# Optimization experiments

Hardware: AMD Instinct MI355X
Metric: run time of the kernel (lower is better)

The kernel has to match this reference:

```python
import jax, jax.numpy as jnp
import numpy as np

D_MODEL = 512
NUM_HEADS = 8


def setup_inputs() -> dict:
    key = jax.random.key(0)
    ks = jax.random.split(key, 12)
    B, S, D = 2, 4096, D_MODEL
    s = 1.0 / np.sqrt(D)
    return {
        "q": jax.random.normal(ks[0], (B, S, D), jnp.float32),
        "k": jax.random.normal(ks[1], (B, S, D), jnp.float32),
        "v": jax.random.normal(ks[2], (B, S, D), jnp.float32),
        "w_q": jax.random.normal(ks[3], (D, D), jnp.float32) * s,
        "b_q": jax.random.normal(ks[4], (D,), jnp.float32) * s,
        "w_k": jax.random.normal(ks[5], (D, D), jnp.float32) * s,
        "b_k": jax.random.normal(ks[6], (D,), jnp.float32) * s,
        "w_v": jax.random.normal(ks[7], (D, D), jnp.float32) * s,
        "b_v": jax.random.normal(ks[8], (D,), jnp.float32) * s,
        "w_o": jax.random.normal(ks[9], (D, D), jnp.float32) * s,
        "b_o": jax.random.normal(ks[10], (D,), jnp.float32) * s,
    }


def _split(x, num_heads):
    B, S, D = x.shape
    return x.reshape(B, S, num_heads, D // num_heads).transpose(0, 2, 1, 3)


def reference(q, k, v, w_q, b_q, w_k, b_k, w_v, b_v, w_o, b_o):
    # Linear projections (torch Linear: x @ W^T + b)
    qp = q @ w_q.T + b_q
    kp = k @ w_k.T + b_k
    vp = v @ w_v.T + b_v
    # split into heads: [B, H, S, d_head]
    qh = _split(qp, NUM_HEADS)
    kh = _split(kp, NUM_HEADS)
    vh = _split(vp, NUM_HEADS)
    d_head = qh.shape[-1]
    # NOTE: original scales by sqrt(d_model of the per-head tensor) == sqrt(d_head)
    score = jnp.einsum("bhqd,bhkd->bhqk", qh, kh) / jnp.sqrt(jnp.float32(d_head))
    attn = jax.nn.softmax(score, axis=-1)  # full [B,H,S,S] materialized, as in source
    out = jnp.einsum("bhqk,bhkd->bhqd", attn, vh)
    # concat heads back to [B, S, D]
    B, H, S, Dh = out.shape
    out = out.transpose(0, 2, 1, 3).reshape(B, S, H * Dh)
    return out @ w_o.T + b_o
```

## Files before the change

kernel.cpp:

```cpp
#include <hip/hip_runtime.h>
#include <math.h>

typedef __bf16 bf16_t;
typedef __bf16 bf16x4_v __attribute__((ext_vector_type(4)));
typedef __bf16 bf16x8_t __attribute__((ext_vector_type(8)));
typedef float f32x4_t __attribute__((ext_vector_type(4)));
typedef unsigned uint2_t __attribute__((ext_vector_type(2)));
typedef unsigned uint4_t __attribute__((ext_vector_type(4)));

#define S_LEN 4096
#define DM 512
#define NH 8
#define DH 64
#define MTOT 8192

#define Q_SCALE 0.1803368801111204f

#define REG   4194304
#define WREG  262144
#define W_OFF (3 * REG)
#define CVT_TOTAL (3 * REG + 4 * WREG)
#define QH_OFF CVT_TOTAL

__device__ inline f32x4_t mfma16(bf16x8_t a, bf16x8_t b, f32x4_t c) {
    return __builtin_amdgcn_mfma_f32_16x16x32_bf16(a, b, c, 0, 0, 0);
}

__device__ inline unsigned pkbf16(float a, float b) {
    unsigned short ra = __builtin_bit_cast(unsigned short, (bf16_t)a);
    unsigned short rb = __builtin_bit_cast(unsigned short, (bf16_t)b);
    return (unsigned)ra | ((unsigned)rb << 16);
}

__device__ inline void async_copy16(const void* g, void* l) {
    __builtin_amdgcn_global_load_lds(
        (const __attribute__((address_space(1))) void*)g,
        (__attribute__((address_space(3))) void*)l, 16, 0, 0);
}

__global__ __launch_bounds__(256) void cvt_all(
    const float* __restrict__ q, const float* __restrict__ k, const float* __restrict__ v,
    const float* __restrict__ wq, const float* __restrict__ wk,
    const float* __restrict__ wv, const float* __restrict__ wo,
    bf16_t* __restrict__ dst)
{
    long gidx = (long)blockIdx.x * 2048 + (long)threadIdx.x * 8;
    const float* src;
    long off = gidx;
    if      (gidx < 1L * REG)          { src = q; }
    else if (gidx < 2L * REG)          { src = k;  off = gidx - 1L * REG; }
    else if (gidx < 3L * REG)          { src = v;  off = gidx - 2L * REG; }
    else if (gidx < W_OFF + 1L * WREG) { src = wq; off = gidx - W_OFF; }
    else if (gidx < W_OFF + 2L * WREG) { src = wk; off = gidx - (W_OFF + 1L * WREG); }
    else if (gidx < W_OFF + 3L * WREG) { src = wv; off = gidx - (W_OFF + 2L * WREG); }
    else                               { src = wo; off = gidx - (W_OFF + 3L * WREG); }
    float4 a = *(const float4*)(src + off);
    float4 b = *(const float4*)(src + off + 4);
    bf16x8_t h;
    h[0] = (bf16_t)a.x; h[1] = (bf16_t)a.y; h[2] = (bf16_t)a.z; h[3] = (bf16_t)a.w;
    h[4] = (bf16_t)b.x; h[5] = (bf16_t)b.y; h[6] = (bf16_t)b.z; h[7] = (bf16_t)b.w;
    *(bf16x8_t*)(dst + gidx) = h;
}

__global__ __launch_bounds__(256) void gemm_qkv(
    const bf16_t* __restrict__ XWb,
    const float* __restrict__ B0, const float* __restrict__ B1, const float* __restrict__ B2,
    bf16_t* __restrict__ dst_base)
{
    const int p = blockIdx.z;
    const bf16_t* __restrict__ X = XWb + (size_t)p * REG;
    const bf16_t* __restrict__ W = XWb + W_OFF + (size_t)p * WREG;
    const float* __restrict__ Bi = (p == 0) ? B0 : ((p == 1) ? B1 : B2);
    bf16_t* __restrict__ dst = dst_base + (size_t)p * REG;

    const int m0 = blockIdx.x * 128;
    const int n0 = blockIdx.y * 128;
    const int tid = threadIdx.x;
    const int lane = tid & 63, wid = tid >> 6;
    const int lm = lane & 15, lg = lane >> 4;
    const int wm = (wid >> 1) * 64, wn = (wid & 1) * 64;

    __shared__ __align__(16) bf16_t As[128 * 64];
    __shared__ __align__(16) bf16_t Bs[128 * 64];

    f32x4_t acc[4][4] = {};

    const int r0 = tid >> 3, c7 = tid & 7;
    const int cA0 = ((lg) ^ (lm & 7)) * 8;
    const int cA1 = ((4 + lg) ^ (lm & 7)) * 8;

    for (int kb = 0; kb < DM / 64; ++kb) {
        const int k0 = kb * 64;
#pragma unroll
        for (int i = 0; i < 4; ++i) {
            int row = i * 32 + r0;
            int ch = c7 ^ (row & 7);
            async_copy16(X + (size_t)(m0 + row) * DM + k0 + ch * 8, (char*)As + (i * 256 + tid) * 16);
            async_copy16(W + (size_t)(n0 + row) * DM + k0 + ch * 8, (char*)Bs + (i * 256 + tid) * 16);
        }
        __syncthreads();
#pragma unroll
        for (int kd = 0; kd < 2; ++kd) {
            const int co = kd ? cA1 : cA0;
            bf16x8_t fa[4], fb[4];
#pragma unroll
            for (int mt = 0; mt < 4; ++mt) {
                fa[mt] = *(const bf16x8_t*)(As + (wm + mt * 16 + lm) * 64 + co);
                fb[mt] = *(const bf16x8_t*)(Bs + (wn + mt * 16 + lm) * 64 + co);
            }
            if (p < 2) {
#pragma unroll
                for (int mt = 0; mt < 4; ++mt)
#pragma unroll
                    for (int nt = 0; nt < 4; ++nt)
                        acc[nt][mt] = mfma16(fb[nt], fa[mt], acc[nt][mt]);
            } else {
#pragma unroll
                for (int mt = 0; mt < 4; ++mt)
#pragma unroll
                    for (int nt = 0; nt < 4; ++nt)
                        acc[mt][nt] = mfma16(fa[mt], fb[nt], acc[mt][nt]);
            }
        }
        __syncthreads();
    }

    if (p == 2) {
#pragma unroll
        for (int nt = 0; nt < 4; ++nt) {
            int col = n0 + wn + nt * 16 + lm;
            float bv = Bi[col];
            int h = (col >> 6) & 7, dc = col & 63;
#pragma unroll
            for (int mt = 0; mt < 4; ++mt) {
                int mrow = m0 + wm + mt * 16 + lg * 4;
                int bb = mrow >> 12, s = mrow & (S_LEN - 1);
                bf16x4_v pk;
#pragma unroll
                for (int r = 0; r < 4; ++r) pk[r] = (bf16_t)(acc[mt][nt][r] + bv);
                *(bf16x4_v*)&dst[(((size_t)(bb * NH + h)) * DH + dc) * S_LEN + s] = pk;
            }
        }
    } else {
        const float scale = (p == 0) ? Q_SCALE : 1.0f;
#pragma unroll
        for (int nt = 0; nt < 4; ++nt) {
            int ncol = n0 + wn + nt * 16 + lg * 4;
            float4 bv4 = *(const float4*)&Bi[ncol];
            int h = (ncol >> 6) & 7, dc = ncol & 63;
#pragma unroll
            for (int mt = 0; mt < 4; ++mt) {
                int m = m0 + wm + mt * 16 + lm;
                int bb = m >> 12, s = m & (S_LEN - 1);
                bf16x4_v pk;
                pk[0] = (bf16_t)((acc[nt][mt][0] + bv4.x) * scale);
                pk[1] = (bf16_t)((acc[nt][mt][1] + bv4.y) * scale);
                pk[2] = (bf16_t)((acc[nt][mt][2] + bv4.z) * scale);
                pk[3] = (bf16_t)((acc[nt][mt][3] + bv4.w) * scale);
                *(bf16x4_v*)&dst[(((size_t)(bb * NH + h)) * S_LEN + s) * DH + dc] = pk;
            }
        }
    }
}

__global__ __launch_bounds__(256, 2) void flash_attn(
    const bf16_t* __restrict__ Qh, const bf16_t* __restrict__ Kh,
    const bf16_t* __restrict__ Vth, bf16_t* __restrict__ O)
{
    const int bh = blockIdx.y;
    const int q0 = blockIdx.x * 128;
    const int tid = threadIdx.x;
    const int lane = tid & 63, wid = tid >> 6;
    const int lm = lane & 15, lg = lane >> 4;
    const int qg = wid & 1;
    const int kvh = wid >> 1;

    const bf16_t* __restrict__ Qb  = Qh  + (size_t)bh * S_LEN * DH;
    const bf16_t* __restrict__ Kb  = Kh  + (size_t)bh * S_LEN * DH;
    const bf16_t* __restrict__ Vtg = Vth + (size_t)bh * S_LEN * DH;

    __shared__ __align__(16) char smem[65536];

    bf16x8_t bQ[4][2];
#pragma unroll
    for (int nt = 0; nt < 4; ++nt)
#pragma unroll
        for (int kd = 0; kd < 2; ++kd)
            bQ[nt][kd] = *(const bf16x8_t*)(Qb + (size_t)(q0 + qg * 64 + nt * 16 + lm) * DH + kd * 32 + lg * 8);

    f32x4_t o_acc[4][4] = {};
    float l_acc[4] = {0.f, 0.f, 0.f, 0.f};

    const int srow = tid >> 3;
    const int slch = (tid & 7) ^ (srow & 7);
    const bf16_t* gK = Kb + (size_t)srow * DH + slch * 8;
    const bf16_t* gV = Vtg + (size_t)srow * S_LEN + slch * 8;

    const int cK0 = ((lg) ^ (lm & 7)) * 16;
    const int cK1 = ((4 + lg) ^ (lm & 7)) * 16;

    {
        char* b = smem;
#pragma unroll
        for (int i = 0; i < 4; ++i)
            async_copy16(gK + (size_t)(32 * i) * DH, b + i * 4096 + tid * 16);
#pragma unroll
        for (int i = 0; i < 4; ++i)
            async_copy16(gV + (size_t)(i & 1) * 32 * S_LEN + (i >> 1) * 64,
                         b + 16384 + i * 4096 + tid * 16);
    }

    const int NT = S_LEN / 128;
    for (int it = 0; it < NT; ++it) {
        const char* buf = smem + (it & 1) * 32768;
        __syncthreads();

        if (it + 1 < NT) {
            char* nb = smem + ((it + 1) & 1) * 32768;
            const int kvb = (it + 1) * 128;
#pragma unroll
            for (int i = 0; i < 4; ++i)
                async_copy16(gK + (size_t)(kvb + 32 * i) * DH, nb + i * 4096 + tid * 16);
#pragma unroll
            for (int i = 0; i < 4; ++i)
                async_copy16(gV + (size_t)(i & 1) * 32 * S_LEN + kvb + (i >> 1) * 64,
                             nb + 16384 + i * 4096 + tid * 16);
        }

        const char* ksb = buf + kvh * 8192;
        const char* vsb = buf + 16384 + kvh * 8192;

        unsigned pk[4][4][2];
#pragma unroll
        for (int mt = 0; mt < 4; ++mt) {
            const char* krow = ksb + (mt * 16 + lm) * 128;
            bf16x8_t aK0 = *(const bf16x8_t*)(krow + cK0);
            bf16x8_t aK1 = *(const bf16x8_t*)(krow + cK1);
#pragma unroll
            for (int nt = 0; nt < 4; ++nt) {
                f32x4_t s = {};
                s = mfma16(aK0, bQ[nt][0], s);
                s = mfma16(aK1, bQ[nt][1], s);
                float e0 = __builtin_amdgcn_exp2f(s[0]);
                float e1 = __builtin_amdgcn_exp2f(s[1]);
                float e2 = __builtin_amdgcn_exp2f(s[2]);
                float e3 = __builtin_amdgcn_exp2f(s[3]);
                pk[mt][nt][0] = pkbf16(e0, e1);
                pk[mt][nt][1] = pkbf16(e2, e3);
                l_acc[nt] += (e0 + e1) + (e2 + e3);
            }
        }

#pragma unroll
        for (int mt = 0; mt < 4; ++mt) {
            const char* vrow = vsb + (mt * 16 + lm) * 128;
#pragma unroll
            for (int cc = 0; cc < 2; ++cc) {
                const int ca = 2 * cc, cb = 2 * cc + 1;
                int pc0 = (ca * 2 + (lg >> 1)) ^ (lm & 7);
                int pc1 = (cb * 2 + (lg >> 1)) ^ (lm & 7);
                uint2_t va0 = *(const uint2_t*)(vrow + pc0 * 16 + (lg & 1) * 8);
                uint2_t va1 = *(const uint2_t*)(vrow + pc1 * 16 + (lg & 1) * 8);
                bf16x8_t vA = __builtin_bit_cast(bf16x8_t, (uint4_t){va0[0], va0[1], va1[0], va1[1]});
#pragma unroll
                for (int nt = 0; nt < 4; ++nt) {
                    bf16x8_t bP = __builtin_bit_cast(bf16x8_t,
                        (uint4_t){pk[ca][nt][0], pk[ca][nt][1], pk[cb][nt][0], pk[cb][nt][1]});
                    o_acc[mt][nt] = mfma16(vA, bP, o_acc[mt][nt]);
                }
            }
        }
    }

#pragma unroll
    for (int nt = 0; nt < 4; ++nt) {
        l_acc[nt] += __shfl_xor(l_acc[nt], 16, 64);
        l_acc[nt] += __shfl_xor(l_acc[nt], 32, 64);
    }

    __syncthreads();

    float* ob = (float*)smem + qg * (64 * 68);
    float* lb = (float*)(smem + 34816);

    if (kvh == 1) {
#pragma unroll
        for (int nt = 0; nt < 4; ++nt) {
#pragma unroll
            for (int mt = 0; mt < 4; ++mt)
                *(f32x4_t*)&ob[(nt * 16 + lm) * 68 + mt * 16 + lg * 4] = o_acc[mt][nt];
            if (lg == 0) lb[qg * 64 + nt * 16 + lm] = l_acc[nt];
        }
    }
    __syncthreads();
    if (kvh == 0) {
        const int bb = bh >> 3, h = bh & 7;
#pragma unroll
        for (int nt = 0; nt < 4; ++nt) {
            float ltot = l_acc[nt] + lb[qg * 64 + nt * 16 + lm];
            float inv = 1.0f / ltot;
            int q = q0 + qg * 64 + nt * 16 + lm;
            size_t base = ((size_t)(bb * S_LEN + q)) * DM + h * DH;
#pragma unroll
            for (int mt = 0; mt < 4; ++mt) {
                f32x4_t orow = *(const f32x4_t*)&ob[(nt * 16 + lm) * 68 + mt * 16 + lg * 4];
                bf16x4_v pkd;
#pragma unroll
                for (int r = 0; r < 4; ++r)
                    pkd[r] = (bf16_t)((o_acc[mt][nt][r] + orow[r]) * inv);
                *(bf16x4_v*)&O[base + mt * 16 + lg * 4] = pkd;
            }
        }
    }
}

__global__ __launch_bounds__(256) void gemm_out(
    const bf16_t* __restrict__ A, const bf16_t* __restrict__ W,
    const float* __restrict__ Bi, float* __restrict__ out)
{
    const int m0 = blockIdx.x * 64;
    const int n0 = blockIdx.y * 128;
    const int tid = threadIdx.x;
    const int lane = tid & 63, wid = tid >> 6;
    const int lm = lane & 15, lg = lane >> 4;
    const int wm = (wid >> 1) * 32, wn = (wid & 1) * 64;

    __shared__ __align__(16) bf16_t As[64 * 64];
    __shared__ __align__(16) bf16_t Bs[128 * 64];

    f32x4_t acc[4][2] = {};

    const int r0 = tid >> 3, c7 = tid & 7;
    const int cA0 = ((lg) ^ (lm & 7)) * 8;
    const int cA1 = ((4 + lg) ^ (lm & 7)) * 8;

    for (int kb = 0; kb < DM / 64; ++kb) {
        const int k0 = kb * 64;
#pragma unroll
        for (int i = 0; i < 2; ++i) {
            int idx = i * 256 + tid;
            int row = idx >> 3;
            int ch = (idx & 7) ^ (row & 7);
            async_copy16(A + (size_t)(m0 + row) * DM + k0 + ch * 8, (char*)As + idx * 16);
        }
#pragma unroll
        for (int i = 0; i < 4; ++i) {
            int row = i * 32 + r0;
            int ch = c7 ^ (row & 7);
            async_copy16(W + (size_t)(n0 + row) * DM + k0 + ch * 8, (char*)Bs + (i * 256 + tid) * 16);
        }
        __syncthreads();
#pragma unroll
        for (int kd = 0; kd < 2; ++kd) {
            const int co = kd ? cA1 : cA0;
            bf16x8_t fa[2], fb[4];
#pragma unroll
            for (int mt = 0; mt < 2; ++mt)
                fa[mt] = *(const bf16x8_t*)(As + (wm + mt * 16 + lm) * 64 + co);
#pragma unroll
            for (int nt = 0; nt < 4; ++nt)
                fb[nt] = *(const bf16x8_t*)(Bs + (wn + nt * 16 + lm) * 64 + co);
#pragma unroll
            for (int nt = 0; nt < 4; ++nt)
#pragma unroll
                for (int mt = 0; mt < 2; ++mt)
                    acc[nt][mt] = mfma16(fb[nt], fa[mt], acc[nt][mt]);
        }
        __syncthreads();
    }

#pragma unroll
    for (int nt = 0; nt < 4; ++nt) {
        int ncol = n0 + wn + nt * 16 + lg * 4;
        float4 bv4 = *(const float4*)&Bi[ncol];
#pragma unroll
        for (int mt = 0; mt < 2; ++mt) {
            int m = m0 + wm + mt * 16 + lm;
            float4 ov;
            ov.x = acc[nt][mt][0] + bv4.x;
            ov.y = acc[nt][mt][1] + bv4.y;
            ov.z = acc[nt][mt][2] + bv4.z;
            ov.w = acc[nt][mt][3] + bv4.w;
            *(float4*)&out[(size_t)m * DM + ncol] = ov;
        }
    }
}

extern "C" void kernel_launch(void* const* d_in, const int* in_sizes, int n_in,
                              void* d_out, int out_size, void* d_ws, size_t ws_size,
                              hipStream_t stream)
{
    const float* q  = (const float*)d_in[0];
    const float* k  = (const float*)d_in[1];
    const float* v  = (const float*)d_in[2];
    const float* wq = (const float*)d_in[3];
    const float* bq = (const float*)d_in[4];
    const float* wk = (const float*)d_in[5];
    const float* bk = (const float*)d_in[6];
    const float* wv = (const float*)d_in[7];
    const float* bv = (const float*)d_in[8];
    const float* wo = (const float*)d_in[9];
    const float* bo = (const float*)d_in[10];
    float* out = (float*)d_out;

    bf16_t* ws = (bf16_t*)d_ws;
    bf16_t* XWb = ws;
    bf16_t* Qh  = ws + QH_OFF;
    bf16_t* Kh  = Qh + REG;
    bf16_t* VTh = Kh + REG;
    bf16_t* Ob  = ws;
    bf16_t* Wob = ws + W_OFF + 3 * (size_t)WREG;

    cvt_all<<<CVT_TOTAL / 2048, 256, 0, stream>>>(q, k, v, wq, wk, wv, wo, XWb);

    dim3 g1(MTOT / 128, DM / 128, 3);
    gemm_qkv<<<g1, 256, 0, stream>>>(XWb, bq, bk, bv, Qh);

    dim3 g2(S_LEN / 128, 2 * NH, 1);
    flash_attn<<<g2, 256, 0, stream>>>(Qh, Kh, VTh, Ob);

    dim3 g3(MTOT / 64, DM / 128, 1);
    gemm_out<<<g3, 256, 0, stream>>>(Ob, Wob, bo, out);
}
```

Measured before the change: 220.2 us.

## Split flash-attention KV tile across eight waves with four-way partial reduction

The flash attention block grows from 256 to 512 threads, so each 128-key tile is split four ways across waves instead of two. Each wave now handles 32 keys per iteration. The partial O accumulators and row sums are combined through a two-stage shared-memory reduction with XOR-swizzled addressing. The aim is more waves per CU and more latency hiding, paid for with extra syncs and reduction traffic at the epilogue and tighter register limits from launch_bounds(512,4).

```diff
diff --git a/kernel.cpp b/kernel.cpp
--- a/kernel.cpp
+++ b/kernel.cpp
@@ -163,7 +163,7 @@
     }
 }
 
-__global__ __launch_bounds__(256, 2) void flash_attn(
+__global__ __launch_bounds__(512, 4) void flash_attn(
     const bf16_t* __restrict__ Qh, const bf16_t* __restrict__ Kh,
     const bf16_t* __restrict__ Vth, bf16_t* __restrict__ O)
 {
@@ -202,12 +202,11 @@
     {
         char* b = smem;
 #pragma unroll
-        for (int i = 0; i < 4; ++i)
-            async_copy16(gK + (size_t)(32 * i) * DH, b + i * 4096 + tid * 16);
-#pragma unroll
-        for (int i = 0; i < 4; ++i)
-            async_copy16(gV + (size_t)(i & 1) * 32 * S_LEN + (i >> 1) * 64,
-                         b + 16384 + i * 4096 + tid * 16);
+        for (int j = 0; j < 2; ++j)
+            async_copy16(gK + (size_t)(j * 64) * DH, b + j * 8192 + tid * 16);
+#pragma unroll
+        for (int i = 0; i < 2; ++i)
+            async_copy16(gV + i * 64, b + 16384 + i * 8192 + tid * 16);
     }
 
     const int NT = S_LEN / 128;
@@ -219,20 +218,20 @@
             char* nb = smem + ((it + 1) & 1) * 32768;
             const int kvb = (it + 1) * 128;
 #pragma unroll
-            for (int i = 0; i < 4; ++i)
-                async_copy16(gK + (size_t)(kvb + 32 * i) * DH, nb + i * 4096 + tid * 16);
-#pragma unroll
-            for (int i = 0; i < 4; ++i)
-                async_copy16(gV + (size_t)(i & 1) * 32 * S_LEN + kvb + (i >> 1) * 64,
-                             nb + 16384 + i * 4096 + tid * 16);
-        }
-
-        const char* ksb = buf + kvh * 8192;
-        const char* vsb = buf + 16384 + kvh * 8192;
-
-        unsigned pk[4][4][2];
-#pragma unroll
-        for (int mt = 0; mt < 4; ++mt) {
+            for (int j = 0; j < 2; ++j)
+                async_copy16(gK + (size_t)(kvb + j * 64) * DH, nb + j * 8192 + tid * 16);
+#pragma unroll
+            for (int i = 0; i < 2; ++i)
+                async_copy16(gV + kvb + i * 64, nb + 16384 + i * 8192 + tid * 16);
+        }
+
+        const char* ksb = buf + kvh * 4096;
+        const char* vsb = buf + 16384 + (kvh >> 1) * 8192;
+        const int qoff = (kvh & 1) * 4;
+
+        unsigned pk[2][4][2];
+#pragma unroll
+        for (int mt = 0; mt < 2; ++mt) {
             const char* krow = ksb + (mt * 16 + lm) * 128;
             bf16x8_t aK0 = *(const bf16x8_t*)(krow + cK0);
             bf16x8_t aK1 = *(const bf16x8_t*)(krow + cK1);
@@ -254,20 +253,16 @@
 #pragma unroll
         for (int mt = 0; mt < 4; ++mt) {
             const char* vrow = vsb + (mt * 16 + lm) * 128;
-#pragma unroll
-            for (int cc = 0; cc < 2; ++cc) {
-                const int ca = 2 * cc, cb = 2 * cc + 1;
-                int pc0 = (ca * 2 + (lg >> 1)) ^ (lm & 7);
-                int pc1 = (cb * 2 + (lg >> 1)) ^ (lm & 7);
-                uint2_t va0 = *(const uint2_t*)(vrow + pc0 * 16 + (lg & 1) * 8);
-                uint2_t va1 = *(const uint2_t*)(vrow + pc1 * 16 + (lg & 1) * 8);
-                bf16x8_t vA = __builtin_bit_cast(bf16x8_t, (uint4_t){va0[0], va0[1], va1[0], va1[1]});
-#pragma unroll
-                for (int nt = 0; nt < 4; ++nt) {
-                    bf16x8_t bP = __builtin_bit_cast(bf16x8_t,
-                        (uint4_t){pk[ca][nt][0], pk[ca][nt][1], pk[cb][nt][0], pk[cb][nt][1]});
-                    o_acc[mt][nt] = mfma16(vA, bP, o_acc[mt][nt]);
-                }
+            int pc0 = (qoff + 0 + (lg >> 1)) ^ (lm & 7);
+            int pc1 = (qoff + 2 + (lg >> 1)) ^ (lm & 7);
+            uint2_t va0 = *(const uint2_t*)(vrow + pc0 * 16 + (lg & 1) * 8);
+            uint2_t va1 = *(const uint2_t*)(vrow + pc1 * 16 + (lg & 1) * 8);
+            bf16x8_t vA = __builtin_bit_cast(bf16x8_t, (uint4_t){va0[0], va0[1], va1[0], va1[1]});
+#pragma unroll
+            for (int nt = 0; nt < 4; ++nt) {
+                bf16x8_t bP = __builtin_bit_cast(bf16x8_t,
+                    (uint4_t){pk[0][nt][0], pk[0][nt][1], pk[1][nt][0], pk[1][nt][1]});
+                o_acc[mt][nt] = mfma16(vA, bP, o_acc[mt][nt]);
             }
         }
     }
@@ -280,34 +275,73 @@
 
     __syncthreads();
 
-    float* ob = (float*)smem + qg * (64 * 68);
-    float* lb = (float*)(smem + 34816);
-
+    float* lbuf = (float*)smem;
+    if (lg == 0) {
+#pragma unroll
+        for (int nt = 0; nt < 4; ++nt)
+            lbuf[(qg * 4 + kvh) * 64 + nt * 16 + lm] = l_acc[nt];
+    }
+    __syncthreads();
+    float inv[4];
+    if (kvh == 0) {
+#pragma unroll
+        for (int nt = 0; nt < 4; ++nt) {
+            int qi = nt * 16 + lm;
+            float lt = lbuf[(qg * 4 + 0) * 64 + qi] + lbuf[(qg * 4 + 1) * 64 + qi]
+                     + lbuf[(qg * 4 + 2) * 64 + qi] + lbuf[(qg * 4 + 3) * 64 + qi];
+            inv[nt] = 1.0f / lt;
+        }
+    }
+    __syncthreads();
+
+    if (kvh >= 2) {
+        char* rb = smem + (qg * 2 + (kvh & 1)) * 16384;
+#pragma unroll
+        for (int nt = 0; nt < 4; ++nt) {
+            int qrow = nt * 16 + lm;
+#pragma unroll
+            for (int mt = 0; mt < 4; ++mt)
+                *(f32x4_t*)(rb + qrow * 256 + (((mt * 4 + lg) ^ (qrow & 7)) * 16)) = o_acc[mt][nt];
+        }
+    }
+    __syncthreads();
+    if (kvh < 2) {
+        const char* rb = smem + (qg * 2 + kvh) * 16384;
+#pragma unroll
+        for (int nt = 0; nt < 4; ++nt) {
+            int qrow = nt * 16 + lm;
+#pragma unroll
+            for (int mt = 0; mt < 4; ++mt)
+                o_acc[mt][nt] += *(const f32x4_t*)(rb + qrow * 256 + (((mt * 4 + lg) ^ (qrow & 7)) * 16));
+        }
+    }
+    __syncthreads();
     if (kvh == 1) {
-#pragma unroll
-        for (int nt = 0; nt < 4; ++nt) {
+        char* rb = smem + (qg * 2 + 1) * 16384;
+#pragma unroll
+        for (int nt = 0; nt < 4; ++nt) {
+            int qrow = nt * 16 + lm;
 #pragma unroll
             for (int mt = 0; mt < 4; ++mt)
-                *(f32x4_t*)&ob[(nt * 16 + lm) * 68 + mt * 16 + lg * 4] = o_acc[mt][nt];
-            if (lg == 0) lb[qg * 64 + nt * 16 + lm] = l_acc[nt];
+                *(f32x4_t*)(rb + qrow * 256 + (((mt * 4 + lg) ^ (qrow & 7)) * 16)) = o_acc[mt][nt];
         }
     }
     __syncthreads();
     if (kvh == 0) {
         const int bb = bh >> 3, h = bh & 7;
-#pragma unroll
-        for (int nt = 0; nt < 4; ++nt) {
-            float ltot = l_acc[nt] + lb[qg * 64 + nt * 16 + lm];
-            float inv = 1.0f / ltot;
-            int q = q0 + qg * 64 + nt * 16 + lm;
+        const char* rb = smem + (qg * 2 + 1) * 16384;
+#pragma unroll
+        for (int nt = 0; nt < 4; ++nt) {
+            int qrow = nt * 16 + lm;
+            int q = q0 + qg * 64 + qrow;
             size_t base = ((size_t)(bb * S_LEN + q)) * DM + h * DH;
 #pragma unroll
             for (int mt = 0; mt < 4; ++mt) {
-                f32x4_t orow = *(const f32x4_t*)&ob[(nt * 16 + lm) * 68 + mt * 16 + lg * 4];
+                f32x4_t part = *(const f32x4_t*)(rb + qrow * 256 + (((mt * 4 + lg) ^ (qrow & 7)) * 16));
                 bf16x4_v pkd;
 #pragma unroll
                 for (int r = 0; r < 4; ++r)
-                    pkd[r] = (bf16_t)((o_acc[mt][nt][r] + orow[r]) * inv);
+                    pkd[r] = (bf16_t)((o_acc[mt][nt][r] + part[r]) * inv[nt]);
                 *(bf16x4_v*)&O[base + mt * 16 + lg * 4] = pkd;
             }
         }
@@ -417,7 +451,7 @@
     gemm_qkv<<<g1, 256, 0, stream>>>(XWb, bq, bk, bv, Qh);
 
     dim3 g2(S_LEN / 128, 2 * NH, 1);
-    flash_attn<<<g2, 256, 0, stream>>>(Qh, Kh, VTh, Ob);
+    flash_attn<<<g2, 512, 0, stream>>>(Qh, Kh, VTh, Ob);
 
     dim3 g3(MTOT / 64, DM / 128, 1);
     gemm_out<<<g3, 256, 0, stream>>>(Ob, Wob, bo, out);
```

Result: slower. 457.2 us (+107.7%).

## Software-pipeline flash attention with 64-key tiles and four-stage smem ring

Applied to the files above, without the earlier changes.

Replaces the double-buffered 128-key loop with a four-slot ring of 64-key K/V tiles. Each iteration overlaps the QK^T and exp of one tile with the PV MFMAs of the previous tile, using two sets of packed probability registers. The aim is to hide the exp and load latency behind matrix work. In exchange it adds twice as many barriers per key and more live registers for the ping-pong probability buffers.

```diff
diff --git a/kernel.cpp b/kernel.cpp
--- a/kernel.cpp
+++ b/kernel.cpp
@@ -163,6 +163,61 @@
     }
 }
 
+__device__ __forceinline__ void stage_kv(
+    char* nb, const bf16_t* gK, const bf16_t* gV, int kvb, int tid)
+{
+    async_copy16(gK + (size_t)kvb * DH, nb + tid * 16);
+    async_copy16(gK + (size_t)(kvb + 32) * DH, nb + 4096 + tid * 16);
+    async_copy16(gV + kvb, nb + 8192 + tid * 16);
+    async_copy16(gV + (size_t)32 * S_LEN + kvb, nb + 12288 + tid * 16);
+}
+
+__device__ __forceinline__ void qk_body(
+    const char* ksb, const bf16x8_t (&bQ)[4][2], int lm, int cK0, int cK1,
+    unsigned (&pk)[2][4][2], float (&l_acc)[4])
+{
+#pragma unroll
+    for (int mt = 0; mt < 2; ++mt) {
+        const char* krow = ksb + (mt * 16 + lm) * 128;
+        bf16x8_t aK0 = *(const bf16x8_t*)(krow + cK0);
+        bf16x8_t aK1 = *(const bf16x8_t*)(krow + cK1);
+#pragma unroll
+        for (int nt = 0; nt < 4; ++nt) {
+            f32x4_t s = {};
+            s = mfma16(aK0, bQ[nt][0], s);
+            s = mfma16(aK1, bQ[nt][1], s);
+            float e0 = __builtin_amdgcn_exp2f(s[0]);
+            float e1 = __builtin_amdgcn_exp2f(s[1]);
+            float e2 = __builtin_amdgcn_exp2f(s[2]);
+            float e3 = __builtin_amdgcn_exp2f(s[3]);
+            pk[mt][nt][0] = pkbf16(e0, e1);
+            pk[mt][nt][1] = pkbf16(e2, e3);
+            l_acc[nt] += (e0 + e1) + (e2 + e3);
+        }
+    }
+}
+
+__device__ __forceinline__ void pv_body(
+    const char* vsb, int lm, int lg, int qoff,
+    const unsigned (&pk)[2][4][2], f32x4_t (&o_acc)[4][4])
+{
+#pragma unroll
+    for (int mt = 0; mt < 4; ++mt) {
+        const char* vrow = vsb + (mt * 16 + lm) * 128;
+        int pc0 = (qoff + 0 + (lg >> 1)) ^ (lm & 7);
+        int pc1 = (qoff + 2 + (lg >> 1)) ^ (lm & 7);
+        uint2_t va0 = *(const uint2_t*)(vrow + pc0 * 16 + (lg & 1) * 8);
+        uint2_t va1 = *(const uint2_t*)(vrow + pc1 * 16 + (lg & 1) * 8);
+        bf16x8_t vA = __builtin_bit_cast(bf16x8_t, (uint4_t){va0[0], va0[1], va1[0], va1[1]});
+#pragma unroll
+        for (int nt = 0; nt < 4; ++nt) {
+            bf16x8_t bP = __builtin_bit_cast(bf16x8_t,
+                (uint4_t){pk[0][nt][0], pk[0][nt][1], pk[1][nt][0], pk[1][nt][1]});
+            o_acc[mt][nt] = mfma16(vA, bP, o_acc[mt][nt]);
+        }
+    }
+}
+
 __global__ __launch_bounds__(256, 2) void flash_attn(
     const bf16_t* __restrict__ Qh, const bf16_t* __restrict__ Kh,
     const bf16_t* __restrict__ Vth, bf16_t* __restrict__ O)
@@ -192,85 +247,40 @@
     float l_acc[4] = {0.f, 0.f, 0.f, 0.f};
 
     const int srow = tid >> 3;
-    const int slch = (tid & 7) ^ (srow & 7);
-    const bf16_t* gK = Kb + (size_t)srow * DH + slch * 8;
-    const bf16_t* gV = Vtg + (size_t)srow * S_LEN + slch * 8;
+    const int sch = (tid & 7) ^ (srow & 7);
+    const bf16_t* gK = Kb + (size_t)srow * DH + sch * 8;
+    const bf16_t* gV = Vtg + (size_t)srow * S_LEN + sch * 8;
 
     const int cK0 = ((lg) ^ (lm & 7)) * 16;
     const int cK1 = ((4 + lg) ^ (lm & 7)) * 16;
-
-    {
-        char* b = smem;
-#pragma unroll
-        for (int i = 0; i < 4; ++i)
-            async_copy16(gK + (size_t)(32 * i) * DH, b + i * 4096 + tid * 16);
-#pragma unroll
-        for (int i = 0; i < 4; ++i)
-            async_copy16(gV + (size_t)(i & 1) * 32 * S_LEN + (i >> 1) * 64,
-                         b + 16384 + i * 4096 + tid * 16);
-    }
-
-    const int NT = S_LEN / 128;
-    for (int it = 0; it < NT; ++it) {
-        const char* buf = smem + (it & 1) * 32768;
-        __syncthreads();
-
-        if (it + 1 < NT) {
-            char* nb = smem + ((it + 1) & 1) * 32768;
-            const int kvb = (it + 1) * 128;
-#pragma unroll
-            for (int i = 0; i < 4; ++i)
-                async_copy16(gK + (size_t)(kvb + 32 * i) * DH, nb + i * 4096 + tid * 16);
-#pragma unroll
-            for (int i = 0; i < 4; ++i)
-                async_copy16(gV + (size_t)(i & 1) * 32 * S_LEN + kvb + (i >> 1) * 64,
-                             nb + 16384 + i * 4096 + tid * 16);
-        }
-
-        const char* ksb = buf + kvh * 8192;
-        const char* vsb = buf + 16384 + kvh * 8192;
-
-        unsigned pk[4][4][2];
-#pragma unroll
-        for (int mt = 0; mt < 4; ++mt) {
-            const char* krow = ksb + (mt * 16 + lm) * 128;
-            bf16x8_t aK0 = *(const bf16x8_t*)(krow + cK0);
-            bf16x8_t aK1 = *(const bf16x8_t*)(krow + cK1);
-#pragma unroll
-            for (int nt = 0; nt < 4; ++nt) {
-                f32x4_t s = {};
-                s = mfma16(aK0, bQ[nt][0], s);
-                s = mfma16(aK1, bQ[nt][1], s);
-                float e0 = __builtin_amdgcn_exp2f(s[0]);
-                float e1 = __builtin_amdgcn_exp2f(s[1]);
-                float e2 = __builtin_amdgcn_exp2f(s[2]);
-                float e3 = __builtin_amdgcn_exp2f(s[3]);
-                pk[mt][nt][0] = pkbf16(e0, e1);
-                pk[mt][nt][1] = pkbf16(e2, e3);
-                l_acc[nt] += (e0 + e1) + (e2 + e3);
-            }
-        }
-
-#pragma unroll
-        for (int mt = 0; mt < 4; ++mt) {
-            const char* vrow = vsb + (mt * 16 + lm) * 128;
-#pragma unroll
-            for (int cc = 0; cc < 2; ++cc) {
-                const int ca = 2 * cc, cb = 2 * cc + 1;
-                int pc0 = (ca * 2 + (lg >> 1)) ^ (lm & 7);
-                int pc1 = (cb * 2 + (lg >> 1)) ^ (lm & 7);
-                uint2_t va0 = *(const uint2_t*)(vrow + pc0 * 16 + (lg & 1) * 8);
-                uint2_t va1 = *(const uint2_t*)(vrow + pc1 * 16 + (lg & 1) * 8);
-                bf16x8_t vA = __builtin_bit_cast(bf16x8_t, (uint4_t){va0[0], va0[1], va1[0], va1[1]});
-#pragma unroll
-                for (int nt = 0; nt < 4; ++nt) {
-                    bf16x8_t bP = __builtin_bit_cast(bf16x8_t,
-                        (uint4_t){pk[ca][nt][0], pk[ca][nt][1], pk[cb][nt][0], pk[cb][nt][1]});
-                    o_acc[mt][nt] = mfma16(vA, bP, o_acc[mt][nt]);
-                }
-            }
-        }
-    }
+    const int qoff = kvh * 4;
+
+    unsigned pk0[2][4][2], pk1[2][4][2];
+
+    stage_kv(smem, gK, gV, 0, tid);
+    stage_kv(smem + 16384, gK, gV, 64, tid);
+
+    __syncthreads();
+    stage_kv(smem + 2 * 16384, gK, gV, 2 * 64, tid);
+    qk_body(smem + kvh * 4096, bQ, lm, cK0, cK1, pk0, l_acc);
+
+    __syncthreads();
+    stage_kv(smem + 3 * 16384, gK, gV, 3 * 64, tid);
+    qk_body(smem + 16384 + kvh * 4096, bQ, lm, cK0, cK1, pk1, l_acc);
+    pv_body(smem + 8192, lm, lg, qoff, pk0, o_acc);
+
+    for (int i = 1; i < 32; ++i) {
+        const int t0 = 2 * i;
+        __syncthreads();
+        if (i < 31) stage_kv(smem + ((t0 + 2) & 3) * 16384, gK, gV, (t0 + 2) * 64, tid);
+        qk_body(smem + (t0 & 3) * 16384 + kvh * 4096, bQ, lm, cK0, cK1, pk0, l_acc);
+        pv_body(smem + ((t0 - 1) & 3) * 16384 + 8192, lm, lg, qoff, pk1, o_acc);
+        __syncthreads();
+        if (i < 31) stage_kv(smem + ((t0 + 3) & 3) * 16384, gK, gV, (t0 + 3) * 64, tid);
+        qk_body(smem + ((t0 + 1) & 3) * 16384 + kvh * 4096, bQ, lm, cK0, cK1, pk1, l_acc);
+        pv_body(smem + (t0 & 3) * 16384 + 8192, lm, lg, qoff, pk0, o_acc);
+    }
+    pv_body(smem + 3 * 16384 + 8192, lm, lg, qoff, pk1, o_acc);
 
 #pragma unroll
     for (int nt = 0; nt < 4; ++nt) {
```

Result: slower. 225.7 us (+2.5%).
